# Kernel tuning notes

Measured on AMD Instinct MI355X. Metric: run time of the kernel, lower is better.

## Reference

```python
import jax, jax.numpy as jnp
import numpy as np

B, S, N, HID = 4, 512, 128, 64


def setup_inputs() -> dict:
    key = jax.random.key(0)
    ks = jax.random.split(key, 32)
    def rn(k, shape, scale=0.1):
        return jax.random.normal(k, shape, dtype=jnp.float32) * scale
    adj = jax.random.randint(ks[0], (N, N), 0, 2).astype(jnp.int32)
    adj = adj.at[jnp.arange(N), jnp.arange(N)].set(1)  # self loops
    inp = {
        'x': jax.random.normal(ks[1], (B, S, N, 1), dtype=jnp.float32),
        'adj': adj,
        'emb_w': rn(ks[2], (1, 16)), 'emb_b': jnp.zeros((16,), jnp.float32),
        'gat1_W': rn(ks[3], (16, 16)), 'gat1_a': rn(ks[4], (32, 1)),
        'gat2_W': rn(ks[5], (16, 8)), 'gat2_a': rn(ks[6], (16, 1)),
        'Wih0': rn(ks[7], (4 * HID, N)), 'Whh0': rn(ks[8], (4 * HID, HID)),
        'bih0': jnp.zeros((4 * HID,), jnp.float32), 'bhh0': jnp.zeros((4 * HID,), jnp.float32),
        'Wih1': rn(ks[9], (4 * HID, HID)), 'Whh1': rn(ks[10], (4 * HID, HID)),
        'bih1': jnp.zeros((4 * HID,), jnp.float32), 'bhh1': jnp.zeros((4 * HID,), jnp.float32),
    }
    comb = HID + 8 * N
    for i, name in enumerate(['dir', 'ret', 'vol']):
        o = 2 if name == 'vol' else 1
        inp[name + '_w1'] = rn(ks[11 + 4 * i], (comb, 32))
        inp[name + '_b1'] = jnp.zeros((32,), jnp.float32)
        inp[name + '_w2'] = rn(ks[12 + 4 * i], (32, o))
        inp[name + '_b2'] = jnp.zeros((o,), jnp.float32)
    return inp


def _gat(h, W, a, mask):
    # e_ij = leakyrelu(a1 . Wh_i + a2 . Wh_j): avoid torch's [M,N,N,2F] concat.
    Wh = h @ W                                  # [M, N, F]
    Fo = W.shape[1]
    f1 = Wh @ a[:Fo]                            # [M, N, 1]
    f2 = Wh @ a[Fo:]                            # [M, N, 1]
    e = jax.nn.leaky_relu(f1 + jnp.swapaxes(f2, 1, 2), 0.2)  # [M, N, N]
    e = jnp.where(mask, e, jnp.float32(-9e15))
    attn = jax.nn.softmax(e, axis=2)
    return attn @ Wh                            # [M, N, F]


def _lstm_layer(xs, Wih, Whh, bih, bhh):
    # xs: [S, B, I]; PyTorch gate order i, f, g, o
    Bsz = xs.shape[1]
    Hd = Whh.shape[1]
    def step(carry, xt):
        h, c = carry
        g = xt @ Wih.T + h @ Whh.T + bih + bhh
        i, f, gg, o = jnp.split(g, 4, axis=-1)
        c = jax.nn.sigmoid(f) * c + jax.nn.sigmoid(i) * jnp.tanh(gg)
        h = jax.nn.sigmoid(o) * jnp.tanh(c)
        return (h, c), h
    init = (jnp.zeros((Bsz, Hd), xs.dtype), jnp.zeros((Bsz, Hd), xs.dtype))
    _, hs = jax.lax.scan(step, init, xs)
    return hs


def reference(x, adj, emb_w, emb_b, gat1_W, gat1_a, gat2_W, gat2_a,
              Wih0, Whh0, bih0, bhh0, Wih1, Whh1, bih1, bhh1,
              dir_w1, dir_b1, dir_w2, dir_b2,
              ret_w1, ret_b1, ret_w2, ret_b2,
              vol_w1, vol_b1, vol_w2, vol_b2):
    Bz, Sz, Nz, _ = x.shape
    mask = (adj > 0)[None]                      # [1, N, N], broadcast over B*S
    xe = (x @ emb_w + emb_b).reshape(Bz * Sz, Nz, 16)
    xg = jax.nn.elu(_gat(xe, gat1_W, gat1_a, mask))   # gat1 concat=True -> elu
    xg = _gat(xg, gat2_W, gat2_a, mask)               # gat2 concat=False
    xg_out = xg.reshape(Bz, Sz, Nz * 8)[:, -1, :]
    xs = jnp.swapaxes(x.reshape(Bz, Sz, Nz), 0, 1)    # [S, B, N]
    hs = _lstm_layer(xs, Wih0, Whh0, bih0, bhh0)
    hs = _lstm_layer(hs, Wih1, Whh1, bih1, bhh1)      # inter-layer dropout off (eval)
    xl_out = hs[-1]                                   # [B, 64]
    c = jnp.concatenate([xl_out, xg_out], axis=1)     # [B, 64 + 8N]
    def head(w1, b1, w2, b2):
        return jax.nn.relu(c @ w1 + b1) @ w2 + b2
    return (head(dir_w1, dir_b1, dir_w2, dir_b2),
            head(ret_w1, ret_b1, ret_w2, ret_b2),
            head(vol_w1, vol_b1, vol_w2, vol_b2))
```

## Files before the change

### kernel.cpp

```cpp
#include <hip/hip_runtime.h>

#define SEQ   512
#define BATCH 4
#define NN    128
#define HID   64
#define G4    256
#define MAGIC 0x13579BDF

typedef _Float16 half2v __attribute__((ext_vector_type(2)));

__device__ __forceinline__ float frcp(float x)  { return __builtin_amdgcn_rcpf(x); }
__device__ __forceinline__ float fsigm(float x) { return frcp(1.f + __expf(-x)); }
__device__ __forceinline__ float ftanh(float x) { return 1.f - 2.f * frcp(1.f + __expf(2.f * x)); }
__device__ __forceinline__ float lrelu(float x) { return x > 0.f ? x : 0.2f * x; }
__device__ __forceinline__ float dot4f(float4 w, float4 h) {
  return fmaf(w.x, h.x, fmaf(w.y, h.y, fmaf(w.z, h.z, w.w * h.w)));
}
__device__ __forceinline__ void pin4(float4& v) {
  asm volatile("" : "+v"(v.x), "+v"(v.y), "+v"(v.z), "+v"(v.w));
}
__device__ __forceinline__ half2v u2h(unsigned u) {
  return __builtin_bit_cast(half2v, u);
}
__device__ __forceinline__ half2v pk16(float lo, float hi) {
  return __builtin_bit_cast(half2v, __builtin_amdgcn_cvt_pkrtz(lo, hi));
}
__device__ __forceinline__ float fdot2(half2v a, half2v b, float c) {
#if __has_builtin(__builtin_amdgcn_fdot2)
  return __builtin_amdgcn_fdot2(a, b, c, false);
#else
  float d = c;
  asm("v_dot2_f32_f16 %0, %1, %2, %0" : "+v"(d) : "v"(a), "v"(b));
  return d;
#endif
}
__device__ __forceinline__ float dot8h(const half2v* w, const uint4& a,
                                       const uint4& b, float acc) {
  acc = fdot2(w[0], u2h(a.x), acc);
  acc = fdot2(w[1], u2h(a.y), acc);
  acc = fdot2(w[2], u2h(a.z), acc);
  acc = fdot2(w[3], u2h(a.w), acc);
  acc = fdot2(w[4], u2h(b.x), acc);
  acc = fdot2(w[5], u2h(b.y), acc);
  acc = fdot2(w[6], u2h(b.z), acc);
  acc = fdot2(w[7], u2h(b.w), acc);
  return acc;
}
__device__ __forceinline__ float nbr1(float x) {
  return __int_as_float(__builtin_amdgcn_update_dpp(
      0, __float_as_int(x), 0xB1, 0xF, 0xF, true));
}

#define BAR_LDS() asm volatile("s_waitcnt lgkmcnt(0)\n\ts_barrier" ::: "memory")

__global__ __attribute__((amdgpu_flat_work_group_size(256, 256),
                          amdgpu_waves_per_eu(1, 4)))
void fused_all(
    const float* __restrict__ x, const int* __restrict__ adj,
    const float* __restrict__ emb_w, const float* __restrict__ emb_b,
    const float* __restrict__ W1, const float* __restrict__ a1,
    const float* __restrict__ W2, const float* __restrict__ a2,
    const float* __restrict__ Wih0, const float* __restrict__ Whh0,
    const float* __restrict__ bih0, const float* __restrict__ bhh0,
    const float* __restrict__ Wih1, const float* __restrict__ Whh1,
    const float* __restrict__ bih1, const float* __restrict__ bhh1,
    const float* __restrict__ dw1, const float* __restrict__ db1,
    const float* __restrict__ dw2, const float* __restrict__ db2,
    const float* __restrict__ rw1, const float* __restrict__ rb1,
    const float* __restrict__ rw2, const float* __restrict__ rb2,
    const float* __restrict__ vw1, const float* __restrict__ vb1,
    const float* __restrict__ vw2, const float* __restrict__ vb2,
    float* __restrict__ X0T, float* __restrict__ xg,
    int* __restrict__ flags, float* __restrict__ out)
{
  const int bid = blockIdx.x;
  const int tid = threadIdx.x;

  if (bid >= 4) {
    const int c = bid - 4;
    __shared__ __align__(16) float xls[NN];
    {
      const int g = tid;
      float4 w4[32];
      {
        const float4* wp = reinterpret_cast<const float4*>(Wih0 + g * NN);
#pragma unroll
        for (int i = 0; i < 32; ++i) w4[i] = wp[i];
#pragma unroll
        for (int i = 0; i < 32; ++i) pin4(w4[i]);
      }
      const float bsum = bih0[g] + bhh0[g];
      for (int phase = 0; phase < 4; ++phase) {
        const int T = c + 128 * phase;
        for (int bb = 0; bb < BATCH; ++bb) {
          if (tid < NN) xls[tid] = x[(bb * SEQ + T) * NN + tid];
          __syncthreads();
          {
            const float4* hp = reinterpret_cast<const float4*>(xls);
            float p0 = 0.f, p1 = 0.f, p2 = 0.f, p3 = 0.f;
#pragma unroll
            for (int k = 0; k < 32; k += 4) {
              p0 += dot4f(w4[k],     hp[k]);
              p1 += dot4f(w4[k + 1], hp[k + 1]);
              p2 += dot4f(w4[k + 2], hp[k + 2]);
              p3 += dot4f(w4[k + 3], hp[k + 3]);
            }
            X0T[(4 * T + bb) * G4 + (g & 63) * 4 + (g >> 6)] =
                ((p0 + p1) + (p2 + p3)) + bsum;
          }
          __syncthreads();
        }
        if (tid == 0 && phase == 0)
          __hip_atomic_store(&flags[c], MAGIC, __ATOMIC_RELEASE,
                             __HIP_MEMORY_SCOPE_AGENT);
        if (tid == 0 && phase == 3)
          __hip_atomic_store(&flags[128 + c], MAGIC, __ATOMIC_RELEASE,
                             __HIP_MEMORY_SCOPE_AGENT);
      }
    }
    if (bid >= 8) return;

    const int b = bid - 4;
    __shared__ float adjm[NN * 129];
    __shared__ __align__(16) float gxls[NN];
    __shared__ float u[16], v[16];
    __shared__ float Wh2[NN][9];
    __shared__ float f1b[NN], f2b[NN];
    __shared__ float p[NN];

    for (int idx = tid; idx < NN * NN; idx += 256)
      adjm[(idx >> 7) * 129 + (idx & 127)] = (adj[idx] > 0) ? 1.f : 0.f;
    if (tid < NN) gxls[tid] = x[(b * SEQ + (SEQ - 1)) * NN + tid];
    if (tid < 16) {
      float uu = 0.f, vv = 0.f;
      for (int fp = 0; fp < 16; ++fp) {
        uu += emb_w[fp] * W1[fp * 16 + tid];
        vv += emb_b[fp] * W1[fp * 16 + tid];
      }
      u[tid] = uu; v[tid] = vv;
    }
    __syncthreads();
    float s1 = 0.f, t1 = 0.f, s2 = 0.f, t2 = 0.f;
    for (int f = 0; f < 16; ++f) {
      s1 += u[f] * a1[f];      t1 += v[f] * a1[f];
      s2 += u[f] * a1[16 + f]; t2 += v[f] * a1[16 + f];
    }
    if (tid < NN) {
      const int i = tid;
      const float f1i = gxls[i] * s1 + t1;
      float m = -1e30f;
      for (int j = 0; j < NN; ++j)
        if (adjm[i * 129 + j] != 0.f)
          m = fmaxf(m, lrelu(f1i + gxls[j] * s2 + t2));
      float ssum = 0.f, ps = 0.f;
      for (int j = 0; j < NN; ++j)
        if (adjm[i * 129 + j] != 0.f) {
          const float wgt = __expf(lrelu(f1i + gxls[j] * s2 + t2) - m);
          ssum += wgt; ps += wgt * gxls[j];
        }
      p[i] = ps / ssum;
    }
    __syncthreads();
    if (tid < NN) {
      const int i = tid;
      float xg1[16];
#pragma unroll
      for (int f = 0; f < 16; ++f) {
        const float ov = p[i] * u[f] + v[f];
        xg1[f] = ov > 0.f ? ov : expm1f(ov);
      }
      float wrow[8];
#pragma unroll
      for (int f2 = 0; f2 < 8; ++f2) wrow[f2] = 0.f;
#pragma unroll
      for (int f = 0; f < 16; ++f) {
        const float xv = xg1[f];
#pragma unroll
        for (int f2 = 0; f2 < 8; ++f2) wrow[f2] += xv * W2[f * 8 + f2];
      }
      float fb1 = 0.f, fb2 = 0.f;
#pragma unroll
      for (int f2 = 0; f2 < 8; ++f2) {
        Wh2[i][f2] = wrow[f2];
        fb1 += wrow[f2] * a2[f2];
        fb2 += wrow[f2] * a2[8 + f2];
      }
      f1b[i] = fb1; f2b[i] = fb2;
    }
    __syncthreads();
    if (tid < NN) {
      const int i = tid;
      const float fi = f1b[i];
      float m = -1e30f;
      for (int j = 0; j < NN; ++j)
        if (adjm[i * 129 + j] != 0.f)
          m = fmaxf(m, lrelu(fi + f2b[j]));
      float ssum = 0.f;
      float o[8];
#pragma unroll
      for (int f2 = 0; f2 < 8; ++f2) o[f2] = 0.f;
      for (int j = 0; j < NN; ++j)
        if (adjm[i * 129 + j] != 0.f) {
          const float wgt = __expf(lrelu(fi + f2b[j]) - m);
          ssum += wgt;
#pragma unroll
          for (int f2 = 0; f2 < 8; ++f2) o[f2] += wgt * Wh2[j][f2];
        }
      const float inv = 1.f / ssum;
#pragma unroll
      for (int f2 = 0; f2 < 8; ++f2)
        xg[b * (NN * 8) + i * 8 + f2] = o[f2] * inv;
    }
    __syncthreads();
    if (tid == 0)
      __hip_atomic_store(&flags[256 + b], MAGIC, __ATOMIC_RELEASE,
                         __HIP_MEMORY_SCOPE_AGENT);
    return;
  }

  const int b   = bid;
  const int t   = tid;
  const int wid = t >> 6;
  const int l   = t & 63;

  __shared__ __align__(16) unsigned hb0[2][32];
  __shared__ __align__(16) unsigned hb1[2][32];
  __shared__ __align__(16) float SBb[2][G4];
  __shared__ float cbuf[1088];
  __shared__ float hidc[96];

  const float* Wsrc = (wid == 0) ? Whh0 : (wid == 1) ? Wih1 : Whh1;
  half2v w[4][32];
  if (wid < 3) {
#pragma unroll
    for (int j = 0; j < 4; ++j) {
      const float* wr = Wsrc + (l + 64 * j) * HID;
#pragma unroll
      for (int c = 0; c < 16; ++c) {
        const float4 wv = *reinterpret_cast<const float4*>(wr + 4 * c);
        w[j][2 * c]     = half2v{(_Float16)wv.x, (_Float16)wv.y};
        w[j][2 * c + 1] = half2v{(_Float16)wv.z, (_Float16)wv.w};
      }
    }
  }
  float4 b1v = make_float4(0.f, 0.f, 0.f, 0.f);
  if (wid == 1) {
    b1v.x = bih1[l]       + bhh1[l];
    b1v.y = bih1[l + 64]  + bhh1[l + 64];
    b1v.z = bih1[l + 128] + bhh1[l + 128];
    b1v.w = bih1[l + 192] + bhh1[l + 192];
  }

  if (t < 64) reinterpret_cast<unsigned*>(hb0)[t] = 0u;
  if (t < 64) reinterpret_cast<unsigned*>(hb1)[t] = 0u;
  float cst0 = 0.f, cst1 = 0.f;
  const float* X0b = X0T + b * G4 + l * 4;

  int c_ok;
  {
    if (t < 32) {
      while (__hip_atomic_fetch_add(&flags[t], 0, __ATOMIC_ACQUIRE,
                                    __HIP_MEMORY_SCOPE_AGENT) != MAGIC) {}
    }
    __syncthreads();
    c_ok = 31;
  }

  float4 xa0 = make_float4(0.f, 0.f, 0.f, 0.f), xa1 = xa0;
  if (wid == 0) {
    xa0 = *reinterpret_cast<const float4*>(X0b + 0 * (BATCH * G4));
    xa1 = *reinterpret_cast<const float4*>(X0b + 1 * (BATCH * G4));
  }

#define LOAD_H8(SRC, RB)                                                       \
  const uint4* hp_ = reinterpret_cast<const uint4*>(&SRC[RB][0]);              \
  const uint4 v0 = hp_[0], v1 = hp_[1], v2 = hp_[2], v3 = hp_[3];              \
  const uint4 v4 = hp_[4], v5 = hp_[5], v6 = hp_[6], v7 = hp_[7]

#define DOT64(G, ACC0)                                                         \
  dot8h(&w[G][24], v6, v7,                                                     \
  dot8h(&w[G][16], v4, v5,                                                     \
  dot8h(&w[G][8],  v2, v3,                                                     \
  dot8h(&w[G][0],  v0, v1, (ACC0)))))

#define PACK_W(DST, WB, HV)                                                    \
  do {                                                                         \
    const float nb_ = nbr1(HV);                                                \
    if ((l & 1) == 0)                                                          \
      DST[WB][l >> 1] = __builtin_bit_cast(unsigned, pk16((HV), nb_));         \
  } while (0)

#define INT_STEP(K, RB, WB, XV)                                                \
  do {                                                                         \
    if (wid == 0) {                                                            \
      if ((K) < SEQ) {                                                         \
        LOAD_H8(hb0, RB);                                                      \
        const float A0 = DOT64(0, 0.f);                                        \
        const float A1 = DOT64(1, 0.f);                                        \
        const float A2 = DOT64(2, 0.f);                                        \
        const float A3 = DOT64(3, 0.f);                                        \
        const float gi = fsigm(A0 + (XV).x);                                   \
        const float gf = fsigm(A1 + (XV).y);                                   \
        const float gg = ftanh(A2 + (XV).z);                                   \
        const float go = fsigm(A3 + (XV).w);                                   \
        cst0 = fmaf(gf, cst0, gi * gg);                                        \
        const float hv = go * ftanh(cst0);                                     \
        PACK_W(hb0, WB, hv);                                                   \
      }                                                                        \
    } else if (wid == 1) {                                                     \
      if ((K) >= 1 && (K) <= SEQ) {                                            \
        LOAD_H8(hb0, RB);                                                      \
        const float B0 = DOT64(0, b1v.x);                                      \
        const float B1 = DOT64(1, b1v.y);                                      \
        const float B2 = DOT64(2, b1v.z);                                      \
        const float B3 = DOT64(3, b1v.w);                                      \
        *reinterpret_cast<float4*>(&SBb[WB][l * 4]) =                          \
            make_float4(B0, B1, B2, B3);                                       \
      }                                                                        \
    } else if (wid == 2) {                                                     \
      if ((K) >= 2) {                                                          \
        LOAD_H8(hb1, RB);                                                      \
        const float C0 = DOT64(0, 0.f);                                        \
        const float C1 = DOT64(1, 0.f);                                        \
        const float C2 = DOT64(2, 0.f);                                        \
        const float C3 = DOT64(3, 0.f);                                        \
        const float4 sb = *reinterpret_cast<const float4*>(&SBb[RB][l * 4]);   \
        const float gi = fsigm(C0 + sb.x);                                     \
        const float gf = fsigm(C1 + sb.y);                                     \
        const float gg = ftanh(C2 + sb.z);                                     \
        const float go = fsigm(C3 + sb.w);                                     \
        cst1 = fmaf(gf, cst1, gi * gg);                                        \
        const float hv = go * ftanh(cst1);                                     \
        PACK_W(hb1, WB, hv);                                                   \
      }                                                                        \
    }                                                                          \
    BAR_LDS();                                                                 \
  } while (0)

  for (int k = 0; k < SEQ + 2; k += 2) {
    if (k + 8 > c_ok && c_ok < 255) {
      const int base = c_ok + 1;
      if (t < 32 && base + t <= 255) {
        while (__hip_atomic_fetch_add(&flags[base + t], 0, __ATOMIC_ACQUIRE,
                                      __HIP_MEMORY_SCOPE_AGENT) != MAGIC) {}
      }
      __syncthreads();
      c_ok = (base + 31 < 255) ? base + 31 : 255;
    }
    if (wid < 3) {
#pragma unroll
      for (int j = 0; j < 4; ++j) {
        half2v* wp = &w[j][0];
        asm volatile("" : "+v"(wp[0]), "+v"(wp[1]), "+v"(wp[2]), "+v"(wp[3]),
                          "+v"(wp[4]), "+v"(wp[5]), "+v"(wp[6]), "+v"(wp[7]));
        asm volatile("" : "+v"(wp[8]), "+v"(wp[9]), "+v"(wp[10]), "+v"(wp[11]),
                          "+v"(wp[12]), "+v"(wp[13]), "+v"(wp[14]), "+v"(wp[15]));
        asm volatile("" : "+v"(wp[16]), "+v"(wp[17]), "+v"(wp[18]), "+v"(wp[19]),
                          "+v"(wp[20]), "+v"(wp[21]), "+v"(wp[22]), "+v"(wp[23]));
        asm volatile("" : "+v"(wp[24]), "+v"(wp[25]), "+v"(wp[26]), "+v"(wp[27]),
                          "+v"(wp[28]), "+v"(wp[29]), "+v"(wp[30]), "+v"(wp[31]));
      }
    }
    float4 xb0 = xa0, xb1 = xa1;
    if (wid == 0 && k + 2 < SEQ) {
      xb0 = *reinterpret_cast<const float4*>(X0b + (k + 2) * (BATCH * G4));
      xb1 = *reinterpret_cast<const float4*>(X0b + (k + 3) * (BATCH * G4));
    }
    INT_STEP(k,     1, 0, xa0);
    INT_STEP(k + 1, 0, 1, xa1);
    xa0 = xb0; xa1 = xb1;
  }
#undef INT_STEP
#undef PACK_W
#undef DOT64
#undef LOAD_H8

  if (t == 0) {
    while (__hip_atomic_fetch_add(&flags[256 + b], 0, __ATOMIC_ACQUIRE,
                                  __HIP_MEMORY_SCOPE_AGENT) != MAGIC) {}
  }
  __syncthreads();

  if (t < 64) {
    const _Float16* hh = reinterpret_cast<const _Float16*>(&hb1[1][0]);
    cbuf[t] = (float)hh[t];
  }
  for (int k = t; k < 1024; k += 256) cbuf[64 + k] = xg[b * 1024 + k];
  __syncthreads();
  if (t < 96) {
    const int head = t >> 5, h = t & 31;
    const float* w1 = (head == 0) ? dw1 : (head == 1) ? rw1 : vw1;
    const float* b1 = (head == 0) ? db1 : (head == 1) ? rb1 : vb1;
    float a0 = 0.f, a1v = 0.f, a2v = 0.f, a3v = 0.f;
    for (int k = 0; k < 1088; k += 4) {
      a0  = fmaf(cbuf[k],     w1[k * 32 + h],       a0);
      a1v = fmaf(cbuf[k + 1], w1[(k + 1) * 32 + h], a1v);
      a2v = fmaf(cbuf[k + 2], w1[(k + 2) * 32 + h], a2v);
      a3v = fmaf(cbuf[k + 3], w1[(k + 3) * 32 + h], a3v);
    }
    hidc[head * 32 + h] = fmaxf(b1[h] + ((a0 + a1v) + (a2v + a3v)), 0.f);
  }
  __syncthreads();
  if (t < 4) {
    const int head2 = (t < 2) ? t : 2;
    const int o = (t < 2) ? 0 : (t - 2);
    const int odim = (t < 2) ? 1 : 2;
    const float* w2  = (head2 == 0) ? dw2 : (head2 == 1) ? rw2 : vw2;
    const float* b2p = (head2 == 0) ? db2 : (head2 == 1) ? rb2 : vb2;
    float acc = b2p[o];
    for (int hh = 0; hh < 32; ++hh)
      acc = fmaf(hidc[head2 * 32 + hh], w2[hh * odim + o], acc);
    const int off = (t == 0) ? b : (t == 1) ? (4 + b) : (8 + 2 * b + o);
    out[off] = acc;
  }
}

extern "C" void kernel_launch(void* const* d_in, const int* in_sizes, int n_in,
                              void* d_out, int out_size, void* d_ws, size_t ws_size,
                              hipStream_t stream) {
  const float* x     = (const float*)d_in[0];
  const int*   adj   = (const int*)  d_in[1];
  const float* emb_w = (const float*)d_in[2];
  const float* emb_b = (const float*)d_in[3];
  const float* g1W   = (const float*)d_in[4];
  const float* g1a   = (const float*)d_in[5];
  const float* g2W   = (const float*)d_in[6];
  const float* g2a   = (const float*)d_in[7];
  const float* Wih0  = (const float*)d_in[8];
  const float* Whh0  = (const float*)d_in[9];
  const float* bih0  = (const float*)d_in[10];
  const float* bhh0  = (const float*)d_in[11];
  const float* Wih1  = (const float*)d_in[12];
  const float* Whh1  = (const float*)d_in[13];
  const float* bih1  = (const float*)d_in[14];
  const float* bhh1  = (const float*)d_in[15];
  const float* dw1 = (const float*)d_in[16]; const float* db1 = (const float*)d_in[17];
  const float* dw2 = (const float*)d_in[18]; const float* db2 = (const float*)d_in[19];
  const float* rw1 = (const float*)d_in[20]; const float* rb1 = (const float*)d_in[21];
  const float* rw2 = (const float*)d_in[22]; const float* rb2 = (const float*)d_in[23];
  const float* vw1 = (const float*)d_in[24]; const float* vb1 = (const float*)d_in[25];
  const float* vw2 = (const float*)d_in[26]; const float* vb2 = (const float*)d_in[27];

  float* ws = (float*)d_ws;
  float* X0 = ws;
  float* xg = ws + SEQ * BATCH * G4;
  int*  flg = (int*)(xg + BATCH * NN * 8);
  float* out = (float*)d_out;

  hipLaunchKernelGGL(fused_all, dim3(132), dim3(256), 0, stream,
                     x, adj, emb_w, emb_b, g1W, g1a, g2W, g2a,
                     Wih0, Whh0, bih0, bhh0, Wih1, Whh1, bih1, bhh1,
                     dw1, db1, dw2, db2, rw1, rb1, rw2, rb2,
                     vw1, vb1, vw2, vb2,
                     X0, xg, flg, out);
}
```

Baseline: 400.6 us.

## Deepen LSTM wave pipeline to 4-slot rings and barrier once per two steps

Enlarges the layer-0 hidden, layer-1 hidden and input-projection LDS buffers to 4-slot rings. Wave 1 now lags wave 0 by two timesteps and wave 2 lags by four, so a single LDS barrier per pair of timesteps is enough instead of one per step. It also drops the DPP neighbour-exchange packing in favour of direct f16 stores, and seeds the dot-product accumulators with the input projection. The aim is to cut barrier latency on the serial recurrence critical path. The cost is a slightly longer pipeline tail and a larger shared-memory footprint.

```diff
diff --git a/kernel.cpp b/kernel.cpp
--- a/kernel.cpp
+++ b/kernel.cpp
@@ -21,9 +21,6 @@
 }
 __device__ __forceinline__ half2v u2h(unsigned u) {
   return __builtin_bit_cast(half2v, u);
-}
-__device__ __forceinline__ half2v pk16(float lo, float hi) {
-  return __builtin_bit_cast(half2v, __builtin_amdgcn_cvt_pkrtz(lo, hi));
 }
 __device__ __forceinline__ float fdot2(half2v a, half2v b, float c) {
 #if __has_builtin(__builtin_amdgcn_fdot2)
@@ -45,10 +42,6 @@
   acc = fdot2(w[6], u2h(b.z), acc);
   acc = fdot2(w[7], u2h(b.w), acc);
   return acc;
-}
-__device__ __forceinline__ float nbr1(float x) {
-  return __int_as_float(__builtin_amdgcn_update_dpp(
-      0, __float_as_int(x), 0xB1, 0xF, 0xF, true));
 }
 
 #define BAR_LDS() asm volatile("s_waitcnt lgkmcnt(0)\n\ts_barrier" ::: "memory")
@@ -223,9 +216,9 @@
   const int wid = t >> 6;
   const int l   = t & 63;
 
-  __shared__ __align__(16) unsigned hb0[2][32];
-  __shared__ __align__(16) unsigned hb1[2][32];
-  __shared__ __align__(16) float SBb[2][G4];
+  __shared__ __align__(16) unsigned hb0[4][32];
+  __shared__ __align__(16) unsigned hb1[4][32];
+  __shared__ __align__(16) float4 SBb[4][64];
   __shared__ float cbuf[1088];
   __shared__ float hidc[96];
 
@@ -251,8 +244,8 @@
     b1v.w = bih1[l + 192] + bhh1[l + 192];
   }
 
-  if (t < 64) reinterpret_cast<unsigned*>(hb0)[t] = 0u;
-  if (t < 64) reinterpret_cast<unsigned*>(hb1)[t] = 0u;
+  if (t < 128) reinterpret_cast<unsigned*>(hb0)[t] = 0u;
+  else         reinterpret_cast<unsigned*>(hb1)[t - 128] = 0u;
   float cst0 = 0.f, cst1 = 0.f;
   const float* X0b = X0T + b * G4 + l * 4;
 
@@ -283,61 +276,54 @@
   dot8h(&w[G][8],  v2, v3,                                                     \
   dot8h(&w[G][0],  v0, v1, (ACC0)))))
 
-#define PACK_W(DST, WB, HV)                                                    \
-  do {                                                                         \
-    const float nb_ = nbr1(HV);                                                \
-    if ((l & 1) == 0)                                                          \
-      DST[WB][l >> 1] = __builtin_bit_cast(unsigned, pk16((HV), nb_));         \
-  } while (0)
-
-#define INT_STEP(K, RB, WB, XV)                                                \
+#define INT_STEP(K, XV)                                                        \
   do {                                                                         \
     if (wid == 0) {                                                            \
       if ((K) < SEQ) {                                                         \
-        LOAD_H8(hb0, RB);                                                      \
-        const float A0 = DOT64(0, 0.f);                                        \
-        const float A1 = DOT64(1, 0.f);                                        \
-        const float A2 = DOT64(2, 0.f);                                        \
-        const float A3 = DOT64(3, 0.f);                                        \
-        const float gi = fsigm(A0 + (XV).x);                                   \
-        const float gf = fsigm(A1 + (XV).y);                                   \
-        const float gg = ftanh(A2 + (XV).z);                                   \
-        const float go = fsigm(A3 + (XV).w);                                   \
+        LOAD_H8(hb0, ((K) - 1) & 3);                                           \
+        const float A0 = DOT64(0, (XV).x);                                     \
+        const float A1 = DOT64(1, (XV).y);                                     \
+        const float A2 = DOT64(2, (XV).z);                                     \
+        const float A3 = DOT64(3, (XV).w);                                     \
+        const float gi = fsigm(A0);                                            \
+        const float gf = fsigm(A1);                                            \
+        const float gg = ftanh(A2);                                            \
+        const float go = fsigm(A3);                                            \
         cst0 = fmaf(gf, cst0, gi * gg);                                        \
         const float hv = go * ftanh(cst0);                                     \
-        PACK_W(hb0, WB, hv);                                                   \
+        reinterpret_cast<_Float16*>(&hb0[(K) & 3][0])[l] = (_Float16)hv;       \
       }                                                                        \
     } else if (wid == 1) {                                                     \
-      if ((K) >= 1 && (K) <= SEQ) {                                            \
-        LOAD_H8(hb0, RB);                                                      \
+      if ((K) >= 2 && (K) <= SEQ + 1) {                                        \
+        const int m_ = (K) - 2;                                                \
+        LOAD_H8(hb0, m_ & 3);                                                  \
         const float B0 = DOT64(0, b1v.x);                                      \
         const float B1 = DOT64(1, b1v.y);                                      \
         const float B2 = DOT64(2, b1v.z);                                      \
         const float B3 = DOT64(3, b1v.w);                                      \
-        *reinterpret_cast<float4*>(&SBb[WB][l * 4]) =                          \
-            make_float4(B0, B1, B2, B3);                                       \
+        SBb[m_ & 3][l] = make_float4(B0, B1, B2, B3);                          \
       }                                                                        \
     } else if (wid == 2) {                                                     \
-      if ((K) >= 2) {                                                          \
-        LOAD_H8(hb1, RB);                                                      \
+      if ((K) >= 4) {                                                          \
+        const int m_ = (K) - 4;                                                \
+        LOAD_H8(hb1, (m_ - 1) & 3);                                            \
         const float C0 = DOT64(0, 0.f);                                        \
         const float C1 = DOT64(1, 0.f);                                        \
         const float C2 = DOT64(2, 0.f);                                        \
         const float C3 = DOT64(3, 0.f);                                        \
-        const float4 sb = *reinterpret_cast<const float4*>(&SBb[RB][l * 4]);   \
+        const float4 sb = SBb[m_ & 3][l];                                      \
         const float gi = fsigm(C0 + sb.x);                                     \
         const float gf = fsigm(C1 + sb.y);                                     \
         const float gg = ftanh(C2 + sb.z);                                     \
         const float go = fsigm(C3 + sb.w);                                     \
         cst1 = fmaf(gf, cst1, gi * gg);                                        \
         const float hv = go * ftanh(cst1);                                     \
-        PACK_W(hb1, WB, hv);                                                   \
+        reinterpret_cast<_Float16*>(&hb1[m_ & 3][0])[l] = (_Float16)hv;        \
       }                                                                        \
     }                                                                          \
-    BAR_LDS();                                                                 \
   } while (0)
 
-  for (int k = 0; k < SEQ + 2; k += 2) {
+  for (int k = 0; k < SEQ + 4; k += 2) {
     if (k + 8 > c_ok && c_ok < 255) {
       const int base = c_ok + 1;
       if (t < 32 && base + t <= 255) {
@@ -366,12 +352,12 @@
       xb0 = *reinterpret_cast<const float4*>(X0b + (k + 2) * (BATCH * G4));
       xb1 = *reinterpret_cast<const float4*>(X0b + (k + 3) * (BATCH * G4));
     }
-    INT_STEP(k,     1, 0, xa0);
-    INT_STEP(k + 1, 0, 1, xa1);
+    INT_STEP(k,     xa0);
+    INT_STEP(k + 1, xa1);
+    BAR_LDS();
     xa0 = xb0; xa1 = xb1;
   }
 #undef INT_STEP
-#undef PACK_W
 #undef DOT64
 #undef LOAD_H8
 
@@ -382,7 +368,7 @@
   __syncthreads();
 
   if (t < 64) {
-    const _Float16* hh = reinterpret_cast<const _Float16*>(&hb1[1][0]);
+    const _Float16* hh = reinterpret_cast<const _Float16*>(&hb1[3][0]);
     cbuf[t] = (float)hh[t];
   }
   for (int k = t; k < 1024; k += 256) cbuf[64 + k] = xg[b * 1024 + k];
```

After: 390.0 us. 1.03x faster.
